# Kernel tuning notes

Hardware: AMD Instinct MI355X
Metric: run time of the kernel (lower is better)

## Reference

```python
import jax, jax.numpy as jnp
import numpy as np

B = 65536
EPS = 1e-5


def _cnot(psi, c, t):
    # psi: [B,2,2,2,2]; qubit q lives on axis q+1. CNOT flips target where control=1.
    c_ax, t_ax = c + 1, t + 1
    p0 = jax.lax.index_in_dim(psi, 0, c_ax, keepdims=True)
    p1 = jax.lax.index_in_dim(psi, 1, c_ax, keepdims=True)
    p1 = jnp.flip(p1, axis=t_ax)
    return jnp.concatenate([p0, p1], axis=c_ax)


def setup_inputs() -> dict:
    key = jax.random.key(0)
    x = jax.random.normal(key, (B, 1, 28, 28), dtype=jnp.float32)
    gamma = jnp.ones((4,), jnp.float32)   # BatchNorm1d(4) weight
    beta = jnp.zeros((4,), jnp.float32)   # BatchNorm1d(4) bias
    return {"x": x, "gamma": gamma, "beta": beta}


def reference(x, gamma, beta):
    bsz = x.shape[0]
    # avg_pool2d(x, 6): kernel=stride=6, no padding -> uses only the top-left 24x24
    pooled = x[:, :, :24, :24].reshape(bsz, 1, 4, 6, 4, 6).mean(axis=(3, 5))
    pooled = pooled.reshape(bsz, 16)
    theta = pooled[:, ::4]  # x[:, i*4] for i=0..3 -> [B,4] RY angles
    half = 0.5 * theta
    q = jnp.stack([jnp.cos(half), jnp.sin(half)], axis=-1)  # [B,4,2], RY|0> amplitudes (real)
    psi = jnp.einsum('bi,bj,bk,bl->bijkl', q[:, 0], q[:, 1], q[:, 2], q[:, 3])
    for c, t in ((0, 1), (1, 2), (2, 3), (3, 0)):
        psi = _cnot(psi, c, t)
    probs = psi * psi  # amplitudes are real
    signs = jnp.array([1.0, -1.0], jnp.float32)
    # <Z_i> = sum_s probs[s] * (-1)^{s_i}
    zs = [jnp.tensordot(probs, signs, axes=[[i + 1], [0]]).sum(axis=(1, 2, 3))
          for i in range(4)]
    out = jnp.stack(zs, axis=1)  # [B,4]
    # BatchNorm1d(4), training mode (biased batch variance)
    mean = out.mean(axis=0)
    var = out.var(axis=0)
    return gamma * (out - mean) / jnp.sqrt(var + EPS) + beta
```

## Files before the change

kernel.cpp:

```cpp
#include <hip/hip_runtime.h>

#define EPS 1e-5f


__global__ __launch_bounds__(256) void qnat_k1(const float* __restrict__ x,
                                               float* __restrict__ z_out,
                                               float* __restrict__ partials,
                                               int bsz) {
    const int t    = threadIdx.x;
    const int lane = t & 63;
    const int w    = t >> 6;
    const int imgBase = blockIdx.x * 16;

    float s1[4] = {0.f, 0.f, 0.f, 0.f};
    float s2[4] = {0.f, 0.f, 0.f, 0.f};

    #pragma unroll
    for (int iter = 0; iter < 4; ++iter) {
        const int img = imgBase + iter * 4 + w;
        float a0 = 0.f, a1 = 0.f, a2 = 0.f, a3 = 0.f;
        if (img < bsz) {
            const float* ip = x + (size_t)img * 784;
            #pragma unroll
            for (int r = 0; r < 3; ++r) {
                const int j = r * 64 + lane;
                if (r < 2 || lane < 40) {
                    const float4 v = *reinterpret_cast<const float4*>(ip + 4 * j);
                    const int m = j % 7;
                    const int p = j / 42;
                    float contrib = 0.f;
                    if (m == 0)      contrib = (v.x + v.y) + (v.z + v.w);
                    else if (m == 1) contrib = v.x + v.y;
                    a0 += (p == 0) ? contrib : 0.f;
                    a1 += (p == 1) ? contrib : 0.f;
                    a2 += (p == 2) ? contrib : 0.f;
                    a3 += (p == 3) ? contrib : 0.f;
                }
            }
        }
        #pragma unroll
        for (int off = 1; off < 64; off <<= 1) {
            a0 += __shfl_xor(a0, off, 64);
            a1 += __shfl_xor(a1, off, 64);
            a2 += __shfl_xor(a2, off, 64);
            a3 += __shfl_xor(a3, off, 64);
        }
        const float k = 1.0f / 36.0f;
        const float c0 = __cosf(a0 * k), c1 = __cosf(a1 * k);
        const float c2 = __cosf(a2 * k), c3 = __cosf(a3 * k);
        const float z1 = c0 * c1;
        const float z2 = z1 * c2;
        const float z3 = z2 * c3;
        const float z0 = c1 * c2 * c3;
        if (img < bsz) {
            if (lane == 0) {
                float4 zz; zz.x = z0; zz.y = z1; zz.z = z2; zz.w = z3;
                *reinterpret_cast<float4*>(z_out + (size_t)img * 4) = zz;
            }
            s1[0] += z0; s1[1] += z1; s1[2] += z2; s1[3] += z3;
            s2[0] += z0 * z0; s2[1] += z1 * z1; s2[2] += z2 * z2; s2[3] += z3 * z3;
        }
    }

    __shared__ float ps[4][8];
    if (lane == 0) {
        #pragma unroll
        for (int k = 0; k < 4; ++k) { ps[w][k] = s1[k]; ps[w][4 + k] = s2[k]; }
    }
    __syncthreads();
    if (t < 8) {
        partials[blockIdx.x * 8 + t] = (ps[0][t] + ps[1][t]) + (ps[2][t] + ps[3][t]);
    }
}

__global__ __launch_bounds__(256) void qnat_k2(const float* __restrict__ z,
                                               const float* __restrict__ partials,
                                               const float* __restrict__ gamma,
                                               const float* __restrict__ beta,
                                               float* __restrict__ out,
                                               int NB, int bsz) {
    __shared__ float red[4][8];
    __shared__ float st[8];

    const int t = threadIdx.x, lane = t & 63, w = t >> 6;

    float acc[8] = {0.f,0.f,0.f,0.f,0.f,0.f,0.f,0.f};
    for (int r = t; r < NB; r += 256) {
        const float4 a = *reinterpret_cast<const float4*>(partials + r * 8);
        const float4 b = *reinterpret_cast<const float4*>(partials + r * 8 + 4);
        acc[0] += a.x; acc[1] += a.y; acc[2] += a.z; acc[3] += a.w;
        acc[4] += b.x; acc[5] += b.y; acc[6] += b.z; acc[7] += b.w;
    }
    #pragma unroll
    for (int off = 1; off < 64; off <<= 1) {
        #pragma unroll
        for (int k = 0; k < 8; ++k) acc[k] += __shfl_xor(acc[k], off, 64);
    }
    if (lane == 0) {
        #pragma unroll
        for (int k = 0; k < 8; ++k) red[w][k] = acc[k];
    }
    __syncthreads();
    if (t < 8) st[t] = (red[0][t] + red[1][t]) + (red[2][t] + red[3][t]);
    __syncthreads();
    if (t < 4) {
        const double invB = 1.0 / (double)bsz;
        const double m   = (double)st[t] * invB;
        const double var = (double)st[4 + t] * invB - m * m;
        st[t]     = (float)m;
        st[4 + t] = gamma[t] * rsqrtf((float)var + EPS);
    }
    __syncthreads();

    const int img = blockIdx.x * 256 + t;
    if (img < bsz) {
        const float4 zv = reinterpret_cast<const float4*>(z)[img];
        float4 o;
        o.x = (zv.x - st[0]) * st[4] + beta[0];
        o.y = (zv.y - st[1]) * st[5] + beta[1];
        o.z = (zv.z - st[2]) * st[6] + beta[2];
        o.w = (zv.w - st[3]) * st[7] + beta[3];
        reinterpret_cast<float4*>(out)[img] = o;
    }
}

extern "C" void kernel_launch(void* const* d_in, const int* in_sizes, int n_in,
                              void* d_out, int out_size, void* d_ws, size_t ws_size,
                              hipStream_t stream) {
    const float* x     = (const float*)d_in[0];
    const float* gamma = (const float*)d_in[1];
    const float* beta  = (const float*)d_in[2];
    float* out = (float*)d_out;

    const int bsz = in_sizes[0] / 784;
    const int NB  = (bsz + 15) / 16;

    float* z        = (float*)d_ws;
    float* partials = (float*)((char*)d_ws + (size_t)bsz * 16);

    qnat_k1<<<NB, 256, 0, stream>>>(x, z, partials, bsz);
    qnat_k2<<<(bsz + 255) / 256, 256, 0, stream>>>(z, partials, gamma, beta, out, NB, bsz);
}
```

Baseline: 42.00 us.

## Map 16 lanes per image with bulk loads and shuffle-transpose reduction

Kernel 1 now gives each image 16 lanes instead of a full wave and issues all 11 float4 loads per lane up front. The previous version looped over 4 images sequentially, each with a 6-step butterfly on 4 values. A short transpose-style shuffle reduction then leaves each lane holding one qubit angle, and the Z products are formed through cross-lane shuffles. Kernel 2 now processes 4 images per thread, which cuts its block count and the repeated reduction of the partials each block performs. The cost is more registers and the extra loads that clamped out-of-range images still issue.

```diff
diff --git a/kernel.cpp b/kernel.cpp
--- a/kernel.cpp
+++ b/kernel.cpp
@@ -10,63 +10,68 @@
     const int t    = threadIdx.x;
     const int lane = t & 63;
     const int w    = t >> 6;
-    const int imgBase = blockIdx.x * 16;
+    const int q    = lane & 15;
+    const int g    = lane >> 4;
+    const int img  = blockIdx.x * 16 + w * 4 + g;
+    const int last = bsz - 1;
+    const int imc  = (img < last) ? img : last;
+    const float* base = x + (size_t)imc * 784 + q * 4;
 
-    float s1[4] = {0.f, 0.f, 0.f, 0.f};
-    float s2[4] = {0.f, 0.f, 0.f, 0.f};
+    float4 v[11];
+    #pragma unroll
+    for (int r = 0; r < 10; ++r)
+        v[r] = *reinterpret_cast<const float4*>(base + r * 64);
+    v[10] = make_float4(0.f, 0.f, 0.f, 0.f);
+    if (q < 8) v[10] = *reinterpret_cast<const float4*>(base + 640);
 
+    float a0 = 0.f, a1 = 0.f, a2 = 0.f, a3 = 0.f;
     #pragma unroll
-    for (int iter = 0; iter < 4; ++iter) {
-        const int img = imgBase + iter * 4 + w;
-        float a0 = 0.f, a1 = 0.f, a2 = 0.f, a3 = 0.f;
-        if (img < bsz) {
-            const float* ip = x + (size_t)img * 784;
-            #pragma unroll
-            for (int r = 0; r < 3; ++r) {
-                const int j = r * 64 + lane;
-                if (r < 2 || lane < 40) {
-                    const float4 v = *reinterpret_cast<const float4*>(ip + 4 * j);
-                    const int m = j % 7;
-                    const int p = j / 42;
-                    float contrib = 0.f;
-                    if (m == 0)      contrib = (v.x + v.y) + (v.z + v.w);
-                    else if (m == 1) contrib = v.x + v.y;
-                    a0 += (p == 0) ? contrib : 0.f;
-                    a1 += (p == 1) ? contrib : 0.f;
-                    a2 += (p == 2) ? contrib : 0.f;
-                    a3 += (p == 3) ? contrib : 0.f;
-                }
-            }
-        }
-        #pragma unroll
-        for (int off = 1; off < 64; off <<= 1) {
-            a0 += __shfl_xor(a0, off, 64);
-            a1 += __shfl_xor(a1, off, 64);
-            a2 += __shfl_xor(a2, off, 64);
-            a3 += __shfl_xor(a3, off, 64);
-        }
-        const float k = 1.0f / 36.0f;
-        const float c0 = __cosf(a0 * k), c1 = __cosf(a1 * k);
-        const float c2 = __cosf(a2 * k), c3 = __cosf(a3 * k);
-        const float z1 = c0 * c1;
-        const float z2 = z1 * c2;
-        const float z3 = z2 * c3;
-        const float z0 = c1 * c2 * c3;
-        if (img < bsz) {
-            if (lane == 0) {
-                float4 zz; zz.x = z0; zz.y = z1; zz.z = z2; zz.w = z3;
-                *reinterpret_cast<float4*>(z_out + (size_t)img * 4) = zz;
-            }
-            s1[0] += z0; s1[1] += z1; s1[2] += z2; s1[3] += z3;
-            s2[0] += z0 * z0; s2[1] += z1 * z1; s2[2] += z2 * z2; s2[3] += z3 * z3;
-        }
+    for (int r = 0; r < 11; ++r) {
+        const int s = r * 16 + q;
+        const int m = s % 7;
+        const int p = s / 42;
+        const float h2 = v[r].x + v[r].y;
+        const float h4 = h2 + v[r].z + v[r].w;
+        const float c  = (m == 0) ? h4 : ((m == 1) ? h2 : 0.f);
+        a0 += (p == 0) ? c : 0.f;
+        a1 += (p == 1) ? c : 0.f;
+        a2 += (p == 2) ? c : 0.f;
+        a3 += (p == 3) ? c : 0.f;
     }
 
+    const bool b0 = (lane & 1) != 0;
+    const bool b1 = (lane & 2) != 0;
+    const int  k  = lane & 3;
+
+    float r0 = __shfl_xor(b0 ? a0 : a1, 1, 64);
+    float u  = (b0 ? a1 : a0) + r0;
+    r0 = __shfl_xor(b0 ? a2 : a3, 1, 64);
+    float vv = (b0 ? a3 : a2) + r0;
+    r0 = __shfl_xor(b1 ? u : vv, 2, 64);
+    float ww = (b1 ? vv : u) + r0;
+    ww += __shfl_xor(ww, 4, 64);
+    ww += __shfl_xor(ww, 8, 64);
+
+    const float c   = __cosf(ww * (1.0f / 36.0f));
+    const float cm1 = __shfl_xor(c, 1, 64);
+    const float cm2 = __shfl_xor(c, 2, 64);
+    const float cm3 = __shfl_xor(cm2, 1, 64);
+    const float t3 = cm2 * cm3, full = cm1 * t3;
+    const float z = (k == 0) ? full : (k == 1) ? c * cm1
+                  : (k == 2) ? c * t3 : c * full;
+
+    const bool valid = (img < bsz);
+    if (valid && q < 4) z_out[(size_t)img * 4 + k] = z;
+
+    float sm1 = (valid && q < 4) ? z : 0.f;
+    float sm2 = sm1 * z;
+    sm1 += __shfl_xor(sm1, 16, 64);
+    sm2 += __shfl_xor(sm2, 16, 64);
+    sm1 += __shfl_xor(sm1, 32, 64);
+    sm2 += __shfl_xor(sm2, 32, 64);
+
     __shared__ float ps[4][8];
-    if (lane == 0) {
-        #pragma unroll
-        for (int k = 0; k < 4; ++k) { ps[w][k] = s1[k]; ps[w][4 + k] = s2[k]; }
-    }
+    if (lane < 4) { ps[w][lane] = sm1; ps[w][4 + lane] = sm2; }
     __syncthreads();
     if (t < 8) {
         partials[blockIdx.x * 8 + t] = (ps[0][t] + ps[1][t]) + (ps[2][t] + ps[3][t]);
@@ -81,7 +86,6 @@
                                                int NB, int bsz) {
     __shared__ float red[4][8];
     __shared__ float st[8];
-
     const int t = threadIdx.x, lane = t & 63, w = t >> 6;
 
     float acc[8] = {0.f,0.f,0.f,0.f,0.f,0.f,0.f,0.f};
@@ -94,11 +98,11 @@
     #pragma unroll
     for (int off = 1; off < 64; off <<= 1) {
         #pragma unroll
-        for (int k = 0; k < 8; ++k) acc[k] += __shfl_xor(acc[k], off, 64);
+        for (int kk = 0; kk < 8; ++kk) acc[kk] += __shfl_xor(acc[kk], off, 64);
     }
     if (lane == 0) {
         #pragma unroll
-        for (int k = 0; k < 8; ++k) red[w][k] = acc[k];
+        for (int kk = 0; kk < 8; ++kk) red[w][kk] = acc[kk];
     }
     __syncthreads();
     if (t < 8) st[t] = (red[0][t] + red[1][t]) + (red[2][t] + red[3][t]);
@@ -112,15 +116,19 @@
     }
     __syncthreads();
 
-    const int img = blockIdx.x * 256 + t;
-    if (img < bsz) {
-        const float4 zv = reinterpret_cast<const float4*>(z)[img];
-        float4 o;
-        o.x = (zv.x - st[0]) * st[4] + beta[0];
-        o.y = (zv.y - st[1]) * st[5] + beta[1];
-        o.z = (zv.z - st[2]) * st[6] + beta[2];
-        o.w = (zv.w - st[3]) * st[7] + beta[3];
-        reinterpret_cast<float4*>(out)[img] = o;
+    const int img0 = blockIdx.x * 1024 + t;
+    #pragma unroll
+    for (int i = 0; i < 4; ++i) {
+        const int img = img0 + i * 256;
+        if (img < bsz) {
+            const float4 zv = reinterpret_cast<const float4*>(z)[img];
+            float4 o;
+            o.x = (zv.x - st[0]) * st[4] + beta[0];
+            o.y = (zv.y - st[1]) * st[5] + beta[1];
+            o.z = (zv.z - st[2]) * st[6] + beta[2];
+            o.w = (zv.w - st[3]) * st[7] + beta[3];
+            reinterpret_cast<float4*>(out)[img] = o;
+        }
     }
 }
 
@@ -134,10 +142,11 @@
 
     const int bsz = in_sizes[0] / 784;
     const int NB  = (bsz + 15) / 16;
+    const int NB2 = (bsz + 1023) / 1024;
 
     float* z        = (float*)d_ws;
     float* partials = (float*)((char*)d_ws + (size_t)bsz * 16);
 
     qnat_k1<<<NB, 256, 0, stream>>>(x, z, partials, bsz);
-    qnat_k2<<<(bsz + 255) / 256, 256, 0, stream>>>(z, partials, gamma, beta, out, NB, bsz);
+    qnat_k2<<<NB2, 256, 0, stream>>>(z, partials, gamma, beta, out, NB, bsz);
 }
```

Result: faster. 39.53 us (-5.9%).
